# Performance work log

Measured on AMD Instinct MI355X. Metric: run time of the kernel, lower is better.

The kernel has to match this reference:

```python
import jax, jax.numpy as jnp
import numpy as np

B, S, K, D, H, COND, MR = 4, 1024, 1024, 1024, 16, 1024, 4
HD = D // H  # 64
INV_SQRT_HD = 1.0 / float(np.sqrt(HD))
GELU_C = 0.7978845608028654  # sqrt(2/pi)


def _make_rope(seqlen):
    pos = jnp.arange(seqlen, dtype=jnp.float32)
    inv = 1.0 / (10000.0 ** (jnp.arange(0, HD // 2, dtype=jnp.float32) * 2.0 / HD))
    ang = pos[:, None] * inv[None, :]                     # [S, HD/2]
    cos = jnp.concatenate([jnp.cos(ang), jnp.cos(ang)], -1)  # [S, HD]
    sin = jnp.concatenate([jnp.sin(ang), jnp.sin(ang)], -1)
    return cos[None, :, None, :], sin[None, :, None, :]   # [1,S,1,HD]


def setup_inputs():
    key = jax.random.key(0)
    ks = jax.random.split(key, 14)
    rn = lambda k, shape, s=0.02: jax.random.normal(k, shape, jnp.float32) * s
    cos_q, sin_q = _make_rope(S)
    cos_k, sin_k = _make_rope(K)
    ada_b = jnp.zeros((6 * D,), jnp.float32)
    ada_b = ada_b.at[2 * D:3 * D].set(0.5).at[5 * D:6 * D].set(0.5)  # gate_msa, gate_mlp init
    return {
        "q_x": jax.random.normal(ks[0], (B, S, D), jnp.float32),
        "kv_x": jax.random.normal(ks[1], (B, K, D), jnp.float32),
        "t_cond": jax.random.normal(ks[2], (B, COND), jnp.float32),
        "cos_q": cos_q, "sin_q": sin_q, "cos_k": cos_k, "sin_k": sin_k,
        "group_idxs": jax.random.randint(ks[3], (B, S), 0, 4, jnp.int32),
        "query_enabled": jax.random.randint(ks[4], (B, S), 0, 2, jnp.int32).astype(bool),
        "qn_w": jnp.ones((D,), jnp.float32),
        "kvn_w": jnp.ones((D,), jnp.float32),
        "n2_w": jnp.ones((D,), jnp.float32),
        "Wq": rn(ks[5], (D, D)), "Wkv": rn(ks[6], (D, 2 * D)), "Wo": rn(ks[7], (D, D)),
        "W1": rn(ks[8], (D, MR * D)), "b1": jnp.zeros((MR * D,), jnp.float32),
        "W2": rn(ks[9], (MR * D, D)), "b2": jnp.zeros((D,), jnp.float32),
        "adaW": rn(ks[10], (COND, 6 * D)), "adab": ada_b,
    }


def layer_norm(x, w):
    mu = jnp.mean(x, -1, keepdims=True)
    var = jnp.var(x, -1, keepdims=True)
    return (x - mu) * jax.lax.rsqrt(var + 1e-5) * w


def rope(x, cos, sin):
    # x: [B,S,H,HD]; cos/sin: [1,S,1,HD]; rotate_half convention
    x1, x2 = jnp.split(x, 2, axis=-1)
    return x * cos + jnp.concatenate([-x2, x1], -1) * sin


def gelu_tanh(x):
    return 0.5 * x * (1.0 + jnp.tanh(GELU_C * (x + 0.044715 * x * x * x)))


def reference(q_x, kv_x, t_cond, cos_q, sin_q, cos_k, sin_k, group_idxs, query_enabled,
              qn_w, kvn_w, n2_w, Wq, Wkv, Wo, W1, b1, W2, b2, adaW, adab):
    # adaLN modulation (inference: dropout disabled -> bias_dropout_add_scale = scale*x + residual)
    mod = (t_cond @ adaW + adab)[:, None, :]               # [B,1,6D]
    sh_msa, sc_msa, g_msa, sh_mlp, sc_mlp, g_mlp = jnp.split(mod, 6, axis=-1)

    qn = layer_norm(q_x, qn_w)
    kvn = layer_norm(kv_x, kvn_w)
    qn = qn * (1.0 + sc_msa) + sh_msa                      # modulate_fused

    q = (qn @ Wq).reshape(B, S, H, HD)
    kv = (kvn @ Wkv).reshape(B, K, 2, H, HD)
    k, v = kv[:, :, 0], kv[:, :, 1]
    q = rope(q, cos_q, sin_q)
    k = rope(k, cos_k, sin_k)

    # group cross-attn mask: attend only where groups differ
    attend = group_idxs[:, :, None] != group_idxs[:, None, :]  # [B,S,K]
    scores = jnp.einsum('bqhd,bkhd->bhqk', q, k) * INV_SQRT_HD
    scores = jnp.where(attend[:, None, :, :], scores, -1e9)
    p = jax.nn.softmax(scores, axis=-1)
    attn = jnp.einsum('bhqk,bkhd->bqhd', p, v).reshape(B, S, D)

    x = g_msa * (attn @ Wo) + q_x                          # fused bias-dropout-add-scale (inference)
    gate = query_enabled[..., None].astype(x.dtype)
    x = x * gate + q_x * (1.0 - gate)                      # gated_update

    x_mid = x
    h = layer_norm(x, n2_w) * (1.0 + sc_mlp) + sh_mlp
    h = gelu_tanh(h @ W1 + b1) @ W2 + b2
    x = g_mlp * h + x_mid
    x = x * gate + x_mid * (1.0 - gate)
    return x
```

## Files before the change

kernel.cpp:

```cpp
#include <hip/hip_runtime.h>
#include <hip/hip_bf16.h>
#include <math.h>

typedef __bf16 bf16_t;
typedef __attribute__((ext_vector_type(8))) __bf16 bf16x8;
typedef __attribute__((ext_vector_type(4))) __bf16 bf16x4;
typedef __attribute__((ext_vector_type(4))) float f32x4;

__global__ __launch_bounds__(256) void mod_init_kernel(
    const float* __restrict__ adab, float* __restrict__ mod)
{
  int i = blockIdx.x * 256 + threadIdx.x;
  int c = i % 6144;
  mod[i] = adab[c];
}

__global__ __launch_bounds__(256) void mod_partial_kernel(
    const float* __restrict__ tc, const float* __restrict__ adaW,
    float* __restrict__ mod)
{
  __shared__ float st[4][128];
  int tid = threadIdx.x, z = blockIdx.y;
  for (int i = tid; i < 512; i += 256)
    st[i >> 7][i & 127] = tc[(i >> 7) * 1024 + z * 128 + (i & 127)];
  __syncthreads();
  int col = blockIdx.x * 256 + tid;
  float a0 = 0.f, a1 = 0.f, a2 = 0.f, a3 = 0.f;
  for (int k = 0; k < 128; ++k) {
    float wv = adaW[(size_t)(z * 128 + k) * 6144 + col];
    a0 = fmaf(st[0][k], wv, a0);
    a1 = fmaf(st[1][k], wv, a1);
    a2 = fmaf(st[2][k], wv, a2);
    a3 = fmaf(st[3][k], wv, a3);
  }
  atomicAdd(&mod[col], a0);
  atomicAdd(&mod[6144 + col], a1);
  atomicAdd(&mod[2 * 6144 + col], a2);
  atomicAdd(&mod[3 * 6144 + col], a3);
}

__global__ __launch_bounds__(256) void transpose_to_bf16(
    const float* __restrict__ in, bf16_t* __restrict__ out, int R, int C)
{
  __shared__ float tile[32][33];
  int c0 = blockIdx.x * 32, r0 = blockIdx.y * 32;
  int tx = threadIdx.x, ty = threadIdx.y;
#pragma unroll
  for (int i = 0; i < 4; ++i)
    tile[ty + i * 8][tx] = in[(size_t)(r0 + ty + i * 8) * C + c0 + tx];
  __syncthreads();
#pragma unroll
  for (int i = 0; i < 4; ++i)
    out[(size_t)(c0 + ty + i * 8) * R + r0 + tx] = (bf16_t)tile[tx][ty + i * 8];
}

__global__ __launch_bounds__(256) void ln_mod_kernel(
    const float* __restrict__ x, const float* __restrict__ wgt,
    const float* __restrict__ mod, int useMod, int shOff, int scOff,
    bf16_t* __restrict__ out)
{
  int row = blockIdx.x;
  int b = row >> 10;
  int tid = threadIdx.x;
  const float* xr = x + (size_t)row * 1024;
  float4 v = ((const float4*)xr)[tid];
  float s = v.x + v.y + v.z + v.w;
  float s2 = v.x * v.x + v.y * v.y + v.z * v.z + v.w * v.w;
#pragma unroll
  for (int off = 32; off > 0; off >>= 1) {
    s += __shfl_down(s, off, 64);
    s2 += __shfl_down(s2, off, 64);
  }
  __shared__ float ps[4], ps2[4];
  if ((tid & 63) == 0) { ps[tid >> 6] = s; ps2[tid >> 6] = s2; }
  __syncthreads();
  float mu = (ps[0] + ps[1] + ps[2] + ps[3]) * (1.0f / 1024.0f);
  float var = (ps2[0] + ps2[1] + ps2[2] + ps2[3]) * (1.0f / 1024.0f) - mu * mu;
  float rs = rsqrtf(var + 1e-5f);
  float xv[4] = {v.x, v.y, v.z, v.w};
#pragma unroll
  for (int i = 0; i < 4; ++i) {
    int col = tid * 4 + i;
    float n = (xv[i] - mu) * rs * wgt[col];
    if (useMod)
      n = n * (1.0f + mod[b * 6144 + scOff + col]) + mod[b * 6144 + shOff + col];
    out[(size_t)row * 1024 + col] = (bf16_t)n;
  }
}

__global__ __launch_bounds__(256) void reduce_q_rope_kernel(
    const bf16_t* __restrict__ P0, const bf16_t* __restrict__ P1,
    const float* __restrict__ cosq, const float* __restrict__ sinq,
    bf16_t* __restrict__ qr)
{
  int t = blockIdx.x * 256 + threadIdx.x;
  int hd = t & 31;
  int h = (t >> 5) & 15;
  int s = (t >> 9) & 1023;
  int b = t >> 19;
  size_t base = ((size_t)(b * 1024 + s)) * 1024 + h * 64 + hd;
  float v1 = (float)P0[base] + (float)P1[base];
  float v2 = (float)P0[base + 32] + (float)P1[base + 32];
  float c1 = cosq[s * 64 + hd], s1 = sinq[s * 64 + hd];
  float c2 = cosq[s * 64 + hd + 32], s2 = sinq[s * 64 + hd + 32];
  float o1 = (v1 * c1 - v2 * s1) * 0.125f;
  float o2 = (v2 * c2 + v1 * s2) * 0.125f;
  size_t ob = ((size_t)(b * 16 + h) * 1024 + s) * 64 + hd;
  qr[ob] = (bf16_t)o1;
  qr[ob + 32] = (bf16_t)o2;
}

__global__ __launch_bounds__(256) void reduce_kv_kernel(
    const bf16_t* __restrict__ P0, const bf16_t* __restrict__ P1,
    const float* __restrict__ cosk, const float* __restrict__ sink,
    bf16_t* __restrict__ kr, bf16_t* __restrict__ vt)
{
  __shared__ float ks[64][65];
  __shared__ float vs[64][65];
  int bh = blockIdx.x;
  int b = bh >> 4, h = bh & 15;
  int n0 = blockIdx.y * 64;
  int tid = threadIdx.x;
#pragma unroll
  for (int it = 0; it < 16; ++it) {
    int linear = tid + it * 256;
    int nl = linear >> 6, hd = linear & 63;
    size_t gi = ((size_t)(b * 1024 + n0 + nl)) * 2048 + h * 64 + hd;
    ks[nl][hd] = (float)P0[gi] + (float)P1[gi];
    vs[hd][nl] = (float)P0[gi + 1024] + (float)P1[gi + 1024];
  }
  __syncthreads();
#pragma unroll
  for (int it = 0; it < 16; ++it) {
    int linear = tid + it * 256;
    int nl = linear >> 6, hd = linear & 63;
    float kv = ks[nl][hd];
    float pv = ks[nl][hd ^ 32];
    float c = cosk[(n0 + nl) * 64 + hd], sn = sink[(n0 + nl) * 64 + hd];
    float o = (hd < 32) ? (kv * c - pv * sn) : (kv * c + pv * sn);
    kr[((size_t)bh * 1024 + n0 + nl) * 64 + hd] = (bf16_t)o;
    int rh = linear >> 6, nn = linear & 63;
    vt[((size_t)bh * 64 + rh) * 1024 + n0 + nn] = (bf16_t)vs[rh][nn];
  }
}

__global__ __launch_bounds__(256, 2) void attn_kernel(
    const bf16_t* __restrict__ qr, const bf16_t* __restrict__ kr,
    const bf16_t* __restrict__ vt, const int* __restrict__ grp,
    bf16_t* __restrict__ outp)
{
  __shared__ bf16_t Ks[64 * 72];
  __shared__ bf16_t Vs[64 * 72];
  __shared__ bf16_t Ps[128 * 72];
  __shared__ int gk[64];
  const int bh = blockIdx.x;
  const int b = bh >> 4, h = bh & 15;
  const int qBase = blockIdx.y * 128;
  const int tid = threadIdx.x, lane = tid & 63, w = tid >> 6;
  const int l15 = lane & 15, l4 = lane >> 4;
  const f32x4 zero = {0.f, 0.f, 0.f, 0.f};

  bf16x8 qA0[2], qA1[2];
  int gqr[2][4];
#pragma unroll
  for (int s = 0; s < 2; ++s) {
    int row = qBase + w * 32 + s * 16;
    const bf16_t* qp = qr + ((size_t)bh * 1024 + row + l15) * 64;
    qA0[s] = *(const bf16x8*)(qp + l4 * 8);
    qA1[s] = *(const bf16x8*)(qp + 32 + l4 * 8);
#pragma unroll
    for (int r = 0; r < 4; ++r) gqr[s][r] = grp[b * 1024 + row + l4 * 4 + r];
  }

  f32x4 oacc[2][4];
  float rsum[2][4];
#pragma unroll
  for (int s = 0; s < 2; ++s)
#pragma unroll
    for (int i = 0; i < 4; ++i) { oacc[s][i] = zero; rsum[s][i] = 0.f; }

  for (int kt = 0; kt < 16; ++kt) {
    __syncthreads();
#pragma unroll
    for (int i = 0; i < 2; ++i) {
      int c = tid * 2 + i;
      int r = c >> 3, cc = (c & 7) * 8;
      *(bf16x8*)(Ks + r * 72 + cc) =
          *(const bf16x8*)(kr + ((size_t)bh * 1024 + kt * 64 + r) * 64 + cc);
      *(bf16x8*)(Vs + r * 72 + cc) =
          *(const bf16x8*)(vt + ((size_t)bh * 64 + r) * 1024 + kt * 64 + cc);
    }
    if (tid < 64) gk[tid] = grp[b * 1024 + kt * 64 + tid];
    __syncthreads();

    int gkv[4];
    bf16x8 kf0[4], kf1[4];
#pragma unroll
    for (int nt = 0; nt < 4; ++nt) {
      gkv[nt] = gk[nt * 16 + l15];
      kf0[nt] = *(const bf16x8*)(Ks + (nt * 16 + l15) * 72 + l4 * 8);
      kf1[nt] = *(const bf16x8*)(Ks + (nt * 16 + l15) * 72 + 32 + l4 * 8);
    }

#pragma unroll
    for (int s = 0; s < 2; ++s) {
      f32x4 sacc[4];
#pragma unroll
      for (int nt = 0; nt < 4; ++nt) sacc[nt] = zero;
#pragma unroll
      for (int nt = 0; nt < 4; ++nt) {
        sacc[nt] = __builtin_amdgcn_mfma_f32_16x16x32_bf16(qA0[s], kf0[nt], sacc[nt], 0, 0, 0);
        sacc[nt] = __builtin_amdgcn_mfma_f32_16x16x32_bf16(qA1[s], kf1[nt], sacc[nt], 0, 0, 0);
      }
#pragma unroll
      for (int r = 0; r < 4; ++r) {
        int gq = gqr[s][r];
        float acc = 0.f;
#pragma unroll
        for (int nt = 0; nt < 4; ++nt) {
          float sv = sacc[nt][r] + ((gq == gkv[nt]) ? -60.f : 0.f);
          float p = __expf(sv);
          acc += p;
          Ps[(w * 32 + s * 16 + l4 * 4 + r) * 72 + nt * 16 + l15] = (bf16_t)p;
        }
        rsum[s][r] += acc;
      }
    }
#pragma unroll
    for (int s = 0; s < 2; ++s) {
      const bf16_t* pp = Ps + (w * 32 + s * 16 + l15) * 72;
      bf16x8 pf0 = *(const bf16x8*)(pp + l4 * 8);
      bf16x8 pf1 = *(const bf16x8*)(pp + 32 + l4 * 8);
#pragma unroll
      for (int nt = 0; nt < 4; ++nt) {
        bf16x8 vf0 = *(const bf16x8*)(Vs + (nt * 16 + l15) * 72 + l4 * 8);
        bf16x8 vf1 = *(const bf16x8*)(Vs + (nt * 16 + l15) * 72 + 32 + l4 * 8);
        oacc[s][nt] = __builtin_amdgcn_mfma_f32_16x16x32_bf16(pf0, vf0, oacc[s][nt], 0, 0, 0);
        oacc[s][nt] = __builtin_amdgcn_mfma_f32_16x16x32_bf16(pf1, vf1, oacc[s][nt], 0, 0, 0);
      }
    }
  }

#pragma unroll
  for (int s = 0; s < 2; ++s)
#pragma unroll
    for (int r = 0; r < 4; ++r) {
      float t = rsum[s][r];
      t += __shfl_xor(t, 1, 64);
      t += __shfl_xor(t, 2, 64);
      t += __shfl_xor(t, 4, 64);
      t += __shfl_xor(t, 8, 64);
      rsum[s][r] = 1.f / t;
    }
#pragma unroll
  for (int s = 0; s < 2; ++s)
#pragma unroll
    for (int r = 0; r < 4; ++r) {
      int srow = qBase + w * 32 + s * 16 + l4 * 4 + r;
      float inv = rsum[s][r];
#pragma unroll
      for (int nt = 0; nt < 4; ++nt)
        outp[((size_t)(b * 1024 + srow)) * 1024 + h * 64 + nt * 16 + l15] =
            (bf16_t)(oacc[s][nt][r] * inv);
    }
}

__device__ __forceinline__ void stage16(const bf16_t* gp, bf16_t* lp) {
  __builtin_amdgcn_global_load_lds(
      (__attribute__((address_space(1))) void*)gp,
      (__attribute__((address_space(3))) void*)lp, 16, 0, 0);
}

template <int EPI>
__global__ __launch_bounds__(256, 2) void gemm_bt(
    const bf16_t* __restrict__ A, const bf16_t* __restrict__ Bt,
    int M, int N, int Kd, int kChunk,
    bf16_t* __restrict__ Cb,
    const float* __restrict__ bias)
{
  __shared__ bf16_t sA[128 * 64];
  __shared__ bf16_t sB[128 * 64];
  const int tid = threadIdx.x;
  const int lane = tid & 63, w = tid >> 6;
  const int wr = w >> 1, wc = w & 1;

  const int gx = gridDim.x, gy = gridDim.y;
  const int L = blockIdx.y * gx + blockIdx.x;
  const int xcd = L & 7, idx = L >> 3;
  const int ry = gy >> 2, rx = gx >> 1;
  const int tileY = (xcd & 3) * ry + (idx % ry);
  const int tileX = (xcd >> 2) * rx + (idx / ry);
  const int rowBase = tileY * 128;
  const int colBase = tileX * 128;

  const int l15 = lane & 15, l4 = lane >> 4;
  const int srow = lane >> 3;
  const int sg = lane & 7;
  const int scol = (sg ^ srow) * 8;
  const int rl = l15 & 7;
  const int g0 = (l4 ^ rl) * 8;
  const int g1 = ((4 + l4) ^ rl) * 8;

  const f32x4 zero = {0.f, 0.f, 0.f, 0.f};
  f32x4 acc[4][4];
#pragma unroll
  for (int i = 0; i < 4; ++i)
#pragma unroll
    for (int j = 0; j < 4; ++j) acc[i][j] = zero;

  const bf16_t* aBase = A + (size_t)(rowBase + w * 32 + srow) * Kd + scol;
  const bf16_t* bBase = Bt + (size_t)(colBase + w * 32 + srow) * Kd + scol;

  const int kStart = blockIdx.z * kChunk;
  for (int k0 = kStart; k0 < kStart + kChunk; k0 += 64) {
    __syncthreads();
#pragma unroll
    for (int i = 0; i < 4; ++i) {
      stage16(aBase + (size_t)i * 8 * Kd + k0, sA + (w * 32 + i * 8) * 64);
      stage16(bBase + (size_t)i * 8 * Kd + k0, sB + (w * 32 + i * 8) * 64);
    }
    __syncthreads();
    bf16x8 af[4], bfr[4];
#pragma unroll
    for (int mt = 0; mt < 4; ++mt)
      af[mt] = *(const bf16x8*)(sA + (wr * 64 + mt * 16 + l15) * 64 + g0);
#pragma unroll
    for (int nt = 0; nt < 4; ++nt)
      bfr[nt] = *(const bf16x8*)(sB + (wc * 64 + nt * 16 + l15) * 64 + g0);
#pragma unroll
    for (int mt = 0; mt < 4; ++mt)
#pragma unroll
      for (int nt = 0; nt < 4; ++nt)
        acc[mt][nt] = __builtin_amdgcn_mfma_f32_16x16x32_bf16(af[mt], bfr[nt],
                                                              acc[mt][nt], 0, 0, 0);
#pragma unroll
    for (int mt = 0; mt < 4; ++mt)
      af[mt] = *(const bf16x8*)(sA + (wr * 64 + mt * 16 + l15) * 64 + g1);
#pragma unroll
    for (int nt = 0; nt < 4; ++nt)
      bfr[nt] = *(const bf16x8*)(sB + (wc * 64 + nt * 16 + l15) * 64 + g1);
#pragma unroll
    for (int mt = 0; mt < 4; ++mt)
#pragma unroll
      for (int nt = 0; nt < 4; ++nt)
        acc[mt][nt] = __builtin_amdgcn_mfma_f32_16x16x32_bf16(af[mt], bfr[nt],
                                                              acc[mt][nt], 0, 0, 0);
  }

  const size_t zOff = (size_t)blockIdx.z * M * N;
#pragma unroll
  for (int mt = 0; mt < 4; ++mt) {
#pragma unroll
    for (int nt = 0; nt < 4; ++nt) {
      int col = colBase + wc * 64 + nt * 16 + l15;
#pragma unroll
      for (int r = 0; r < 4; ++r) {
        int rr = rowBase + wr * 64 + mt * 16 + l4 * 4 + r;
        float v = acc[mt][nt][r];
        if constexpr (EPI == 1) {
          float t = v + bias[col];
          float z = 0.7978845608028654f * (t + 0.044715f * t * t * t);
          float e = __expf(2.f * z);
          float g = 0.5f * t * (2.f - 2.f / (e + 1.f));
          Cb[(size_t)rr * N + col] = (bf16_t)g;
        } else {
          Cb[zOff + (size_t)rr * N + col] = (bf16_t)v;
        }
      }
    }
  }
}

__global__ __launch_bounds__(256) void ln2_fused_kernel(
    const bf16_t* __restrict__ P0, const bf16_t* __restrict__ P1,
    const float* __restrict__ qx, const float* __restrict__ n2w,
    const float* __restrict__ mod, const int* __restrict__ qen,
    float* __restrict__ xbuf, bf16_t* __restrict__ xnmod)
{
  int row = blockIdx.x;
  int b = row >> 10;
  int tid = threadIdx.x;
  bool en = qen[row] != 0;
  bf16x4 p0 = *(const bf16x4*)(P0 + (size_t)row * 1024 + tid * 4);
  bf16x4 p1 = *(const bf16x4*)(P1 + (size_t)row * 1024 + tid * 4);
  float4 res = ((const float4*)(qx + (size_t)row * 1024))[tid];
  float4 g = ((const float4*)(mod + b * 6144 + 2048))[tid];
  float4 x;
  x.x = en ? fmaf(g.x, (float)p0[0] + (float)p1[0], res.x) : res.x;
  x.y = en ? fmaf(g.y, (float)p0[1] + (float)p1[1], res.y) : res.y;
  x.z = en ? fmaf(g.z, (float)p0[2] + (float)p1[2], res.z) : res.z;
  x.w = en ? fmaf(g.w, (float)p0[3] + (float)p1[3], res.w) : res.w;
  ((float4*)(xbuf + (size_t)row * 1024))[tid] = x;

  float s = x.x + x.y + x.z + x.w;
  float s2 = x.x * x.x + x.y * x.y + x.z * x.z + x.w * x.w;
#pragma unroll
  for (int off = 32; off > 0; off >>= 1) {
    s += __shfl_down(s, off, 64);
    s2 += __shfl_down(s2, off, 64);
  }
  __shared__ float ps[4], ps2[4];
  if ((tid & 63) == 0) { ps[tid >> 6] = s; ps2[tid >> 6] = s2; }
  __syncthreads();
  float mu = (ps[0] + ps[1] + ps[2] + ps[3]) * (1.0f / 1024.0f);
  float var = (ps2[0] + ps2[1] + ps2[2] + ps2[3]) * (1.0f / 1024.0f) - mu * mu;
  float rs = rsqrtf(var + 1e-5f);
  float4 sc = ((const float4*)(mod + b * 6144 + 4096))[tid];
  float4 sh = ((const float4*)(mod + b * 6144 + 3072))[tid];
  float4 wv = ((const float4*)n2w)[tid];
  float xv[4] = {x.x, x.y, x.z, x.w};
  float scv[4] = {sc.x, sc.y, sc.z, sc.w};
  float shv[4] = {sh.x, sh.y, sh.z, sh.w};
  float wvv[4] = {wv.x, wv.y, wv.z, wv.w};
#pragma unroll
  for (int i = 0; i < 4; ++i) {
    float n = (xv[i] - mu) * rs * wvv[i];
    n = n * (1.0f + scv[i]) + shv[i];
    xnmod[(size_t)row * 1024 + tid * 4 + i] = (bf16_t)n;
  }
}

__global__ __launch_bounds__(256) void final_reduce_kernel(
    const bf16_t* __restrict__ P, const float* __restrict__ b2,
    const float* __restrict__ mod, const int* __restrict__ qen,
    const float* __restrict__ xbuf, float* __restrict__ out)
{
  int row = blockIdx.x;
  int b = row >> 10;
  int tid = threadIdx.x;
  bool en = qen[row] != 0;
  size_t ro = (size_t)row * 1024 + tid * 4;
  bf16x4 p0 = *(const bf16x4*)(P + ro);
  bf16x4 p1 = *(const bf16x4*)(P + 4194304 + ro);
  bf16x4 p2 = *(const bf16x4*)(P + 2 * 4194304 + ro);
  bf16x4 p3 = *(const bf16x4*)(P + 3 * 4194304 + ro);
  float4 bb = ((const float4*)b2)[tid];
  float4 xm = *(const float4*)(xbuf + ro);
  float4 g = ((const float4*)(mod + b * 6144 + 5120))[tid];
  float4 o;
  float v0 = (float)p0[0] + (float)p1[0] + (float)p2[0] + (float)p3[0] + bb.x;
  float v1 = (float)p0[1] + (float)p1[1] + (float)p2[1] + (float)p3[1] + bb.y;
  float v2 = (float)p0[2] + (float)p1[2] + (float)p2[2] + (float)p3[2] + bb.z;
  float v3 = (float)p0[3] + (float)p1[3] + (float)p2[3] + (float)p3[3] + bb.w;
  o.x = en ? fmaf(g.x, v0, xm.x) : xm.x;
  o.y = en ? fmaf(g.y, v1, xm.y) : xm.y;
  o.z = en ? fmaf(g.z, v2, xm.z) : xm.z;
  o.w = en ? fmaf(g.w, v3, xm.w) : xm.w;
  *(float4*)(out + ro) = o;
}

extern "C" void kernel_launch(void* const* d_in, const int* in_sizes, int n_in,
                              void* d_out, int out_size, void* d_ws, size_t ws_size,
                              hipStream_t stream)
{
  const float* q_x    = (const float*)d_in[0];
  const float* kv_x   = (const float*)d_in[1];
  const float* t_cond = (const float*)d_in[2];
  const float* cos_q  = (const float*)d_in[3];
  const float* sin_q  = (const float*)d_in[4];
  const float* cos_k  = (const float*)d_in[5];
  const float* sin_k  = (const float*)d_in[6];
  const int*   grp    = (const int*)d_in[7];
  const int*   qen    = (const int*)d_in[8];
  const float* qn_w   = (const float*)d_in[9];
  const float* kvn_w  = (const float*)d_in[10];
  const float* n2_w   = (const float*)d_in[11];
  const float* Wq     = (const float*)d_in[12];
  const float* Wkv    = (const float*)d_in[13];
  const float* Wo     = (const float*)d_in[14];
  const float* W1     = (const float*)d_in[15];
  const float* b1     = (const float*)d_in[16];
  const float* W2     = (const float*)d_in[17];
  const float* b2     = (const float*)d_in[18];
  const float* adaW   = (const float*)d_in[19];
  const float* adab   = (const float*)d_in[20];
  float* out = (float*)d_out;

  char* ws = (char*)d_ws;
  const size_t MB = 1ull << 20;
  float*  mod    = (float*)(ws + 0);
  bf16_t* Wq_t   = (bf16_t*)(ws + 98304);
  bf16_t* Wkv_t  = (bf16_t*)(ws + 98304 + 2 * MB);
  bf16_t* Wo_t   = (bf16_t*)(ws + 98304 + 6 * MB);
  bf16_t* W1_t   = (bf16_t*)(ws + 98304 + 8 * MB);
  bf16_t* W2_t   = (bf16_t*)(ws + 98304 + 16 * MB);
  bf16_t* qn_mod = (bf16_t*)(ws + 98304 + 24 * MB);
  bf16_t* kvn    = (bf16_t*)(ws + 98304 + 32 * MB);
  bf16_t* q_r    = (bf16_t*)(ws + 98304 + 40 * MB);
  bf16_t* k_r    = (bf16_t*)(ws + 98304 + 48 * MB);
  bf16_t* v_t    = (bf16_t*)(ws + 98304 + 56 * MB);
  bf16_t* h1     = (bf16_t*)(ws + 98304 + 64 * MB);
  bf16_t* scr    = (bf16_t*)(ws + 98304 + 96 * MB);
  bf16_t* xn_mod = qn_mod;
  bf16_t* attn_o = kvn;
  float*  xbuf   = (float*)q_r;

  mod_init_kernel<<<96, 256, 0, stream>>>(adab, mod);
  mod_partial_kernel<<<dim3(24, 8), 256, 0, stream>>>(t_cond, adaW, mod);
  transpose_to_bf16<<<dim3(32, 32),  dim3(32, 8), 0, stream>>>(Wq,  Wq_t,  1024, 1024);
  transpose_to_bf16<<<dim3(64, 32),  dim3(32, 8), 0, stream>>>(Wkv, Wkv_t, 1024, 2048);
  transpose_to_bf16<<<dim3(32, 32),  dim3(32, 8), 0, stream>>>(Wo,  Wo_t,  1024, 1024);
  transpose_to_bf16<<<dim3(128, 32), dim3(32, 8), 0, stream>>>(W1,  W1_t,  1024, 4096);
  transpose_to_bf16<<<dim3(32, 128), dim3(32, 8), 0, stream>>>(W2,  W2_t,  4096, 1024);
  ln_mod_kernel<<<4096, 256, 0, stream>>>(q_x,  qn_w,  mod, 1, 0, 1024, qn_mod);
  ln_mod_kernel<<<4096, 256, 0, stream>>>(kv_x, kvn_w, mod, 0, 0, 0,    kvn);
  gemm_bt<4><<<dim3(8, 32, 2), 256, 0, stream>>>(qn_mod, Wq_t, 4096, 1024, 1024, 512,
                                                 scr, nullptr);
  reduce_q_rope_kernel<<<8192, 256, 0, stream>>>(scr, scr + 4194304, cos_q, sin_q, q_r);
  gemm_bt<4><<<dim3(16, 32, 2), 256, 0, stream>>>(kvn, Wkv_t, 4096, 2048, 1024, 512,
                                                  scr, nullptr);
  reduce_kv_kernel<<<dim3(64, 16), 256, 0, stream>>>(scr, scr + 8388608, cos_k, sin_k,
                                                     k_r, v_t);
  attn_kernel<<<dim3(64, 8), 256, 0, stream>>>(q_r, k_r, v_t, grp, attn_o);
  gemm_bt<4><<<dim3(8, 32, 2), 256, 0, stream>>>(attn_o, Wo_t, 4096, 1024, 1024, 512,
                                                 scr, nullptr);
  ln2_fused_kernel<<<4096, 256, 0, stream>>>(scr, scr + 4194304, q_x, n2_w, mod, qen,
                                             xbuf, xn_mod);
  gemm_bt<1><<<dim3(32, 32, 1), 256, 0, stream>>>(xn_mod, W1_t, 4096, 4096, 1024, 1024,
                                                  h1, b1);
  gemm_bt<4><<<dim3(8, 32, 4), 256, 0, stream>>>(h1, W2_t, 4096, 1024, 4096, 1024,
                                                 scr, nullptr);
  final_reduce_kernel<<<4096, 256, 0, stream>>>(scr, b2, mod, qen, xbuf, out);
}
```

Measured before the change: 436.5 us.

## Compact enabled query rows and skip post-attention GEMMs for disabled rows

Adds a compaction kernel that builds an index list of rows with query_enabled set. The Wo projection gathers only those rows, and the LN2 and MLP GEMMs run on the compacted rows, with blocks past the live count exiting early. Disabled rows are copied straight from q_x into the output. The change also merges the five weight transposes and the two layer norms into single launches and changes the Wo split-K to 4. The intent is to avoid GEMM work on rows whose result is discarded, at the cost of a serial single-block scan and an indirect row gather.

After: 397.3 us. 1.1x faster.

```diff
diff --git a/kernel.cpp b/kernel.cpp
--- a/kernel.cpp
+++ b/kernel.cpp
@@ -7,12 +7,51 @@
 typedef __attribute__((ext_vector_type(4))) __bf16 bf16x4;
 typedef __attribute__((ext_vector_type(4))) float f32x4;
 
+__global__ __launch_bounds__(256) void compact_kernel(
+    const int* __restrict__ qen, int* __restrict__ idx, int* __restrict__ McPtr)
+{
+  __shared__ int cnts[256];
+  int t = threadIdx.x;
+  int flags[16], c = 0;
+#pragma unroll
+  for (int i = 0; i < 16; ++i) {
+    flags[i] = qen[t * 16 + i] != 0;
+    c += flags[i];
+  }
+  cnts[t] = c;
+  __syncthreads();
+  for (int off = 1; off < 256; off <<= 1) {
+    int v = cnts[t];
+    if (t >= off) v += cnts[t - off];
+    __syncthreads();
+    cnts[t] = v;
+    __syncthreads();
+  }
+  int p = cnts[t] - c;
+  int total = cnts[255];
+#pragma unroll
+  for (int i = 0; i < 16; ++i)
+    if (flags[i]) idx[p++] = t * 16 + i;
+  if (t == 0) *McPtr = total;
+  for (int j = total + t; j < 4096; j += 256) idx[j] = 0;
+}
+
+__global__ __launch_bounds__(256) void copy_disabled_kernel(
+    const int* __restrict__ qen, const float* __restrict__ qx,
+    float* __restrict__ out)
+{
+  int row = blockIdx.x;
+  if (qen[row]) return;
+  int tid = threadIdx.x;
+  ((float4*)(out + (size_t)row * 1024))[tid] =
+      ((const float4*)(qx + (size_t)row * 1024))[tid];
+}
+
 __global__ __launch_bounds__(256) void mod_init_kernel(
     const float* __restrict__ adab, float* __restrict__ mod)
 {
   int i = blockIdx.x * 256 + threadIdx.x;
-  int c = i % 6144;
-  mod[i] = adab[c];
+  mod[i] = adab[i % 6144];
 }
 
 __global__ __launch_bounds__(256) void mod_partial_kernel(
@@ -39,11 +78,23 @@
   atomicAdd(&mod[3 * 6144 + col], a3);
 }
 
-__global__ __launch_bounds__(256) void transpose_to_bf16(
-    const float* __restrict__ in, bf16_t* __restrict__ out, int R, int C)
+__global__ __launch_bounds__(256) void transpose_all(
+    const float* __restrict__ Wq, const float* __restrict__ Wkv,
+    const float* __restrict__ Wo, const float* __restrict__ W1,
+    const float* __restrict__ W2,
+    bf16_t* __restrict__ oWq, bf16_t* __restrict__ oWkv,
+    bf16_t* __restrict__ oWo, bf16_t* __restrict__ oW1,
+    bf16_t* __restrict__ oW2)
 {
   __shared__ float tile[32][33];
-  int c0 = blockIdx.x * 32, r0 = blockIdx.y * 32;
+  int bid = blockIdx.x;
+  const float* in; bf16_t* out; int R, C, gx, local;
+  if (bid < 1024)      { in = Wq;  out = oWq;  R = 1024; C = 1024; gx = 32;  local = bid; }
+  else if (bid < 3072) { in = Wkv; out = oWkv; R = 1024; C = 2048; gx = 64;  local = bid - 1024; }
+  else if (bid < 4096) { in = Wo;  out = oWo;  R = 1024; C = 1024; gx = 32;  local = bid - 3072; }
+  else if (bid < 8192) { in = W1;  out = oW1;  R = 1024; C = 4096; gx = 128; local = bid - 4096; }
+  else                 { in = W2;  out = oW2;  R = 4096; C = 1024; gx = 32;  local = bid - 8192; }
+  int c0 = (local % gx) * 32, r0 = (local / gx) * 32;
   int tx = threadIdx.x, ty = threadIdx.y;
 #pragma unroll
   for (int i = 0; i < 4; ++i)
@@ -54,16 +105,22 @@
     out[(size_t)(c0 + ty + i * 8) * R + r0 + tx] = (bf16_t)tile[tx][ty + i * 8];
 }
 
-__global__ __launch_bounds__(256) void ln_mod_kernel(
-    const float* __restrict__ x, const float* __restrict__ wgt,
-    const float* __restrict__ mod, int useMod, int shOff, int scOff,
-    bf16_t* __restrict__ out)
-{
-  int row = blockIdx.x;
+__global__ __launch_bounds__(256) void ln_both_kernel(
+    const float* __restrict__ qx, const float* __restrict__ kvx,
+    const float* __restrict__ qnw, const float* __restrict__ kvnw,
+    const float* __restrict__ mod,
+    bf16_t* __restrict__ qn_out, bf16_t* __restrict__ kvn_out)
+{
+  int rowg = blockIdx.x;
+  bool isQ = rowg < 4096;
+  int row = isQ ? rowg : rowg - 4096;
   int b = row >> 10;
   int tid = threadIdx.x;
-  const float* xr = x + (size_t)row * 1024;
-  float4 v = ((const float4*)xr)[tid];
+  const float* x = (isQ ? qx : kvx) + (size_t)row * 1024;
+  const float* wgt = isQ ? qnw : kvnw;
+  bf16_t* outp = (isQ ? qn_out : kvn_out) + (size_t)row * 1024;
+
+  float4 v = ((const float4*)x)[tid];
   float s = v.x + v.y + v.z + v.w;
   float s2 = v.x * v.x + v.y * v.y + v.z * v.z + v.w * v.w;
 #pragma unroll
@@ -82,9 +139,9 @@
   for (int i = 0; i < 4; ++i) {
     int col = tid * 4 + i;
     float n = (xv[i] - mu) * rs * wgt[col];
-    if (useMod)
-      n = n * (1.0f + mod[b * 6144 + scOff + col]) + mod[b * 6144 + shOff + col];
-    out[(size_t)row * 1024 + col] = (bf16_t)n;
+    if (isQ)
+      n = n * (1.0f + mod[b * 6144 + 1024 + col]) + mod[b * 6144 + col];
+    outp[col] = (bf16_t)n;
   }
 }
 
@@ -139,8 +196,7 @@
     float c = cosk[(n0 + nl) * 64 + hd], sn = sink[(n0 + nl) * 64 + hd];
     float o = (hd < 32) ? (kv * c - pv * sn) : (kv * c + pv * sn);
     kr[((size_t)bh * 1024 + n0 + nl) * 64 + hd] = (bf16_t)o;
-    int rh = linear >> 6, nn = linear & 63;
-    vt[((size_t)bh * 64 + rh) * 1024 + n0 + nn] = (bf16_t)vs[rh][nn];
+    vt[((size_t)bh * 64 + nl) * 1024 + n0 + hd] = (bf16_t)vs[nl][hd];
   }
 }
 
@@ -271,12 +327,9 @@
       (__attribute__((address_space(3))) void*)lp, 16, 0, 0);
 }
 
-template <int EPI>
-__global__ __launch_bounds__(256, 2) void gemm_bt(
+__global__ __launch_bounds__(256, 2) void gemm_bt_full(
     const bf16_t* __restrict__ A, const bf16_t* __restrict__ Bt,
-    int M, int N, int Kd, int kChunk,
-    bf16_t* __restrict__ Cb,
-    const float* __restrict__ bias)
+    int M, int N, int Kd, int kChunk, bf16_t* __restrict__ Cb)
 {
   __shared__ bf16_t sA[128 * 64];
   __shared__ bf16_t sB[128 * 64];
@@ -286,10 +339,10 @@
 
   const int gx = gridDim.x, gy = gridDim.y;
   const int L = blockIdx.y * gx + blockIdx.x;
-  const int xcd = L & 7, idx = L >> 3;
+  const int xcd = L & 7, id2 = L >> 3;
   const int ry = gy >> 2, rx = gx >> 1;
-  const int tileY = (xcd & 3) * ry + (idx % ry);
-  const int tileX = (xcd >> 2) * rx + (idx / ry);
+  const int tileY = (xcd & 3) * ry + (id2 % ry);
+  const int tileX = (xcd >> 2) * rx + (id2 / ry);
   const int rowBase = tileY * 128;
   const int colBase = tileX * 128;
 
@@ -349,7 +402,103 @@
 
   const size_t zOff = (size_t)blockIdx.z * M * N;
 #pragma unroll
-  for (int mt = 0; mt < 4; ++mt) {
+  for (int mt = 0; mt < 4; ++mt)
+#pragma unroll
+    for (int nt = 0; nt < 4; ++nt) {
+      int col = colBase + wc * 64 + nt * 16 + l15;
+#pragma unroll
+      for (int r = 0; r < 4; ++r) {
+        int rr = rowBase + wr * 64 + mt * 16 + l4 * 4 + r;
+        Cb[zOff + (size_t)rr * N + col] = (bf16_t)acc[mt][nt][r];
+      }
+    }
+}
+
+template <int EPI, int GATHER>
+__global__ __launch_bounds__(256, 2) void gemm_bt_c(
+    const bf16_t* __restrict__ A, const bf16_t* __restrict__ Bt,
+    int N, int Kd, int kChunk, bf16_t* __restrict__ Cb,
+    const float* __restrict__ bias,
+    const int* __restrict__ idxG, const int* __restrict__ McPtr)
+{
+  __shared__ bf16_t sA[128 * 64];
+  __shared__ bf16_t sB[128 * 64];
+  const int Mc = *McPtr;
+  const int gx = gridDim.x;
+  const int L = blockIdx.y * gx + blockIdx.x;
+  const int xcd = L & 7, id2 = L >> 3;
+  const int tileY = (id2 / gx) * 8 + xcd;
+  const int tileX = id2 % gx;
+  const int rowBase = tileY * 128;
+  if (rowBase >= Mc) return;
+  const int colBase = tileX * 128;
+
+  const int tid = threadIdx.x;
+  const int lane = tid & 63, w = tid >> 6;
+  const int wr = w >> 1, wc = w & 1;
+  const int l15 = lane & 15, l4 = lane >> 4;
+  const int srow = lane >> 3;
+  const int sg = lane & 7;
+  const int scol = (sg ^ srow) * 8;
+  const int rl = l15 & 7;
+  const int g0 = (l4 ^ rl) * 8;
+  const int g1 = ((4 + l4) ^ rl) * 8;
+
+  const f32x4 zero = {0.f, 0.f, 0.f, 0.f};
+  f32x4 acc[4][4];
+#pragma unroll
+  for (int i = 0; i < 4; ++i)
+#pragma unroll
+    for (int j = 0; j < 4; ++j) acc[i][j] = zero;
+
+  const bf16_t* aB[4];
+#pragma unroll
+  for (int i = 0; i < 4; ++i) {
+    int rowc = rowBase + w * 32 + i * 8 + srow;
+    int arow = GATHER ? idxG[rowc] : rowc;
+    aB[i] = A + (size_t)arow * Kd + scol;
+  }
+  const bf16_t* bBase = Bt + (size_t)(colBase + w * 32 + srow) * Kd + scol;
+
+  const int kStart = blockIdx.z * kChunk;
+  for (int k0 = kStart; k0 < kStart + kChunk; k0 += 64) {
+    __syncthreads();
+#pragma unroll
+    for (int i = 0; i < 4; ++i) {
+      stage16(aB[i] + k0, sA + (w * 32 + i * 8) * 64);
+      stage16(bBase + (size_t)i * 8 * Kd + k0, sB + (w * 32 + i * 8) * 64);
+    }
+    __syncthreads();
+    bf16x8 af[4], bfr[4];
+#pragma unroll
+    for (int mt = 0; mt < 4; ++mt)
+      af[mt] = *(const bf16x8*)(sA + (wr * 64 + mt * 16 + l15) * 64 + g0);
+#pragma unroll
+    for (int nt = 0; nt < 4; ++nt)
+      bfr[nt] = *(const bf16x8*)(sB + (wc * 64 + nt * 16 + l15) * 64 + g0);
+#pragma unroll
+    for (int mt = 0; mt < 4; ++mt)
+#pragma unroll
+      for (int nt = 0; nt < 4; ++nt)
+        acc[mt][nt] = __builtin_amdgcn_mfma_f32_16x16x32_bf16(af[mt], bfr[nt],
+                                                              acc[mt][nt], 0, 0, 0);
+#pragma unroll
+    for (int mt = 0; mt < 4; ++mt)
+      af[mt] = *(const bf16x8*)(sA + (wr * 64 + mt * 16 + l15) * 64 + g1);
+#pragma unroll
+    for (int nt = 0; nt < 4; ++nt)
+      bfr[nt] = *(const bf16x8*)(sB + (wc * 64 + nt * 16 + l15) * 64 + g1);
+#pragma unroll
+    for (int mt = 0; mt < 4; ++mt)
+#pragma unroll
+      for (int nt = 0; nt < 4; ++nt)
+        acc[mt][nt] = __builtin_amdgcn_mfma_f32_16x16x32_bf16(af[mt], bfr[nt],
+                                                              acc[mt][nt], 0, 0, 0);
+  }
+
+  const size_t zOff = (size_t)blockIdx.z * 4096 * N;
+#pragma unroll
+  for (int mt = 0; mt < 4; ++mt)
 #pragma unroll
     for (int nt = 0; nt < 4; ++nt) {
       int col = colBase + wc * 64 + nt * 16 + l15;
@@ -368,29 +517,32 @@
         }
       }
     }
-  }
 }
 
 __global__ __launch_bounds__(256) void ln2_fused_kernel(
-    const bf16_t* __restrict__ P0, const bf16_t* __restrict__ P1,
-    const float* __restrict__ qx, const float* __restrict__ n2w,
-    const float* __restrict__ mod, const int* __restrict__ qen,
-    float* __restrict__ xbuf, bf16_t* __restrict__ xnmod)
-{
-  int row = blockIdx.x;
-  int b = row >> 10;
+    const bf16_t* __restrict__ P, const float* __restrict__ qx,
+    const float* __restrict__ n2w, const float* __restrict__ mod,
+    const int* __restrict__ idxG, const int* __restrict__ McPtr,
+    float* __restrict__ xbufc, bf16_t* __restrict__ xnc)
+{
+  int rowc = blockIdx.x;
+  if (rowc >= *McPtr) return;
+  int rr = idxG[rowc];
+  int b = rr >> 10;
   int tid = threadIdx.x;
-  bool en = qen[row] != 0;
-  bf16x4 p0 = *(const bf16x4*)(P0 + (size_t)row * 1024 + tid * 4);
-  bf16x4 p1 = *(const bf16x4*)(P1 + (size_t)row * 1024 + tid * 4);
-  float4 res = ((const float4*)(qx + (size_t)row * 1024))[tid];
+  size_t rc = (size_t)rowc * 1024 + tid * 4;
+  bf16x4 p0 = *(const bf16x4*)(P + rc);
+  bf16x4 p1 = *(const bf16x4*)(P + 4194304 + rc);
+  bf16x4 p2 = *(const bf16x4*)(P + 2 * 4194304 + rc);
+  bf16x4 p3 = *(const bf16x4*)(P + 3 * 4194304 + rc);
+  float4 res = ((const float4*)(qx + (size_t)rr * 1024))[tid];
   float4 g = ((const float4*)(mod + b * 6144 + 2048))[tid];
   float4 x;
-  x.x = en ? fmaf(g.x, (float)p0[0] + (float)p1[0], res.x) : res.x;
-  x.y = en ? fmaf(g.y, (float)p0[1] + (float)p1[1], res.y) : res.y;
-  x.z = en ? fmaf(g.z, (float)p0[2] + (float)p1[2], res.z) : res.z;
-  x.w = en ? fmaf(g.w, (float)p0[3] + (float)p1[3], res.w) : res.w;
-  ((float4*)(xbuf + (size_t)row * 1024))[tid] = x;
+  x.x = fmaf(g.x, (float)p0[0] + (float)p1[0] + (float)p2[0] + (float)p3[0], res.x);
+  x.y = fmaf(g.y, (float)p0[1] + (float)p1[1] + (float)p2[1] + (float)p3[1], res.y);
+  x.z = fmaf(g.z, (float)p0[2] + (float)p1[2] + (float)p2[2] + (float)p3[2], res.z);
+  x.w = fmaf(g.w, (float)p0[3] + (float)p1[3] + (float)p2[3] + (float)p3[3], res.w);
+  *(float4*)(xbufc + rc) = x;
 
   float s = x.x + x.y + x.z + x.w;
   float s2 = x.x * x.x + x.y * x.y + x.z * x.z + x.w * x.w;
@@ -416,37 +568,39 @@
   for (int i = 0; i < 4; ++i) {
     float n = (xv[i] - mu) * rs * wvv[i];
     n = n * (1.0f + scv[i]) + shv[i];
-    xnmod[(size_t)row * 1024 + tid * 4 + i] = (bf16_t)n;
+    xnc[(size_t)rowc * 1024 + tid * 4 + i] = (bf16_t)n;
   }
 }
 
 __global__ __launch_bounds__(256) void final_reduce_kernel(
     const bf16_t* __restrict__ P, const float* __restrict__ b2,
-    const float* __restrict__ mod, const int* __restrict__ qen,
-    const float* __restrict__ xbuf, float* __restrict__ out)
-{
-  int row = blockIdx.x;
-  int b = row >> 10;
+    const float* __restrict__ mod, const int* __restrict__ idxG,
+    const int* __restrict__ McPtr, const float* __restrict__ xbufc,
+    float* __restrict__ out)
+{
+  int rowc = blockIdx.x;
+  if (rowc >= *McPtr) return;
+  int rr = idxG[rowc];
+  int b = rr >> 10;
   int tid = threadIdx.x;
-  bool en = qen[row] != 0;
-  size_t ro = (size_t)row * 1024 + tid * 4;
-  bf16x4 p0 = *(const bf16x4*)(P + ro);
-  bf16x4 p1 = *(const bf16x4*)(P + 4194304 + ro);
-  bf16x4 p2 = *(const bf16x4*)(P + 2 * 4194304 + ro);
-  bf16x4 p3 = *(const bf16x4*)(P + 3 * 4194304 + ro);
+  size_t rc = (size_t)rowc * 1024 + tid * 4;
+  bf16x4 p0 = *(const bf16x4*)(P + rc);
+  bf16x4 p1 = *(const bf16x4*)(P + 4194304 + rc);
+  bf16x4 p2 = *(const bf16x4*)(P + 2 * 4194304 + rc);
+  bf16x4 p3 = *(const bf16x4*)(P + 3 * 4194304 + rc);
   float4 bb = ((const float4*)b2)[tid];
-  float4 xm = *(const float4*)(xbuf + ro);
+  float4 xm = *(const float4*)(xbufc + rc);
   float4 g = ((const float4*)(mod + b * 6144 + 5120))[tid];
-  float4 o;
   float v0 = (float)p0[0] + (float)p1[0] + (float)p2[0] + (float)p3[0] + bb.x;
   float v1 = (float)p0[1] + (float)p1[1] + (float)p2[1] + (float)p3[1] + bb.y;
   float v2 = (float)p0[2] + (float)p1[2] + (float)p2[2] + (float)p3[2] + bb.z;
   float v3 = (float)p0[3] + (float)p1[3] + (float)p2[3] + (float)p3[3] + bb.w;
-  o.x = en ? fmaf(g.x, v0, xm.x) : xm.x;
-  o.y = en ? fmaf(g.y, v1, xm.y) : xm.y;
-  o.z = en ? fmaf(g.z, v2, xm.z) : xm.z;
-  o.w = en ? fmaf(g.w, v3, xm.w) : xm.w;
-  *(float4*)(out + ro) = o;
+  float4 o;
+  o.x = fmaf(g.x, v0, xm.x);
+  o.y = fmaf(g.y, v1, xm.y);
+  o.z = fmaf(g.z, v2, xm.z);
+  o.w = fmaf(g.w, v3, xm.w);
+  *(float4*)(out + (size_t)rr * 1024 + tid * 4) = o;
 }
 
 extern "C" void kernel_launch(void* const* d_in, const int* in_sizes, int n_in,
@@ -479,46 +633,48 @@
   char* ws = (char*)d_ws;
   const size_t MB = 1ull << 20;
   float*  mod    = (float*)(ws + 0);
-  bf16_t* Wq_t   = (bf16_t*)(ws + 98304);
-  bf16_t* Wkv_t  = (bf16_t*)(ws + 98304 + 2 * MB);
-  bf16_t* Wo_t   = (bf16_t*)(ws + 98304 + 6 * MB);
-  bf16_t* W1_t   = (bf16_t*)(ws + 98304 + 8 * MB);
-  bf16_t* W2_t   = (bf16_t*)(ws + 98304 + 16 * MB);
-  bf16_t* qn_mod = (bf16_t*)(ws + 98304 + 24 * MB);
-  bf16_t* kvn    = (bf16_t*)(ws + 98304 + 32 * MB);
-  bf16_t* q_r    = (bf16_t*)(ws + 98304 + 40 * MB);
-  bf16_t* k_r    = (bf16_t*)(ws + 98304 + 48 * MB);
-  bf16_t* v_t    = (bf16_t*)(ws + 98304 + 56 * MB);
-  bf16_t* h1     = (bf16_t*)(ws + 98304 + 64 * MB);
-  bf16_t* scr    = (bf16_t*)(ws + 98304 + 96 * MB);
-  bf16_t* xn_mod = qn_mod;
+  int*    idxL   = (int*)(ws + 98304);
+  int*    McPtr  = (int*)(ws + 98304 + 16384);
+  char*   wbase  = ws + 131072;
+  bf16_t* Wq_t   = (bf16_t*)(wbase);
+  bf16_t* Wkv_t  = (bf16_t*)(wbase + 2 * MB);
+  bf16_t* Wo_t   = (bf16_t*)(wbase + 6 * MB);
+  bf16_t* W1_t   = (bf16_t*)(wbase + 8 * MB);
+  bf16_t* W2_t   = (bf16_t*)(wbase + 16 * MB);
+  bf16_t* qn_mod = (bf16_t*)(wbase + 24 * MB);
+  bf16_t* kvn    = (bf16_t*)(wbase + 32 * MB);
+  bf16_t* q_r    = (bf16_t*)(wbase + 40 * MB);
+  bf16_t* k_r    = (bf16_t*)(wbase + 48 * MB);
+  bf16_t* v_t    = (bf16_t*)(wbase + 56 * MB);
+  bf16_t* h1     = (bf16_t*)(wbase + 64 * MB);
+  bf16_t* scr    = (bf16_t*)(wbase + 96 * MB);
+  bf16_t* xn_c   = qn_mod;
   bf16_t* attn_o = kvn;
-  float*  xbuf   = (float*)q_r;
-
+  float*  xbuf_c = (float*)q_r;
+
+  compact_kernel<<<1, 256, 0, stream>>>(qen, idxL, McPtr);
+  copy_disabled_kernel<<<4096, 256, 0, stream>>>(qen, q_x, out);
   mod_init_kernel<<<96, 256, 0, stream>>>(adab, mod);
   mod_partial_kernel<<<dim3(24, 8), 256, 0, stream>>>(t_cond, adaW, mod);
-  transpose_to_bf16<<<dim3(32, 32),  dim3(32, 8), 0, stream>>>(Wq,  Wq_t,  1024, 1024);
-  transpose_to_bf16<<<dim3(64, 32),  dim3(32, 8), 0, stream>>>(Wkv, Wkv_t, 1024, 2048);
-  transpose_to_bf16<<<dim3(32, 32),  dim3(32, 8), 0, stream>>>(Wo,  Wo_t,  1024, 1024);
-  transpose_to_bf16<<<dim3(128, 32), dim3(32, 8), 0, stream>>>(W1,  W1_t,  1024, 4096);
-  transpose_to_bf16<<<dim3(32, 128), dim3(32, 8), 0, stream>>>(W2,  W2_t,  4096, 1024);
-  ln_mod_kernel<<<4096, 256, 0, stream>>>(q_x,  qn_w,  mod, 1, 0, 1024, qn_mod);
-  ln_mod_kernel<<<4096, 256, 0, stream>>>(kv_x, kvn_w, mod, 0, 0, 0,    kvn);
-  gemm_bt<4><<<dim3(8, 32, 2), 256, 0, stream>>>(qn_mod, Wq_t, 4096, 1024, 1024, 512,
-                                                 scr, nullptr);
+  transpose_all<<<12288, dim3(32, 8), 0, stream>>>(Wq, Wkv, Wo, W1, W2,
+                                                   Wq_t, Wkv_t, Wo_t, W1_t, W2_t);
+  ln_both_kernel<<<8192, 256, 0, stream>>>(q_x, kv_x, qn_w, kvn_w, mod,
+                                           qn_mod, kvn);
+  gemm_bt_full<<<dim3(8, 32, 2), 256, 0, stream>>>(qn_mod, Wq_t, 4096, 1024, 1024,
+                                                   512, scr);
   reduce_q_rope_kernel<<<8192, 256, 0, stream>>>(scr, scr + 4194304, cos_q, sin_q, q_r);
-  gemm_bt<4><<<dim3(16, 32, 2), 256, 0, stream>>>(kvn, Wkv_t, 4096, 2048, 1024, 512,
-                                                  scr, nullptr);
+  gemm_bt_full<<<dim3(16, 32, 2), 256, 0, stream>>>(kvn, Wkv_t, 4096, 2048, 1024,
+                                                    512, scr);
   reduce_kv_kernel<<<dim3(64, 16), 256, 0, stream>>>(scr, scr + 8388608, cos_k, sin_k,
                                                      k_r, v_t);
   attn_kernel<<<dim3(64, 8), 256, 0, stream>>>(q_r, k_r, v_t, grp, attn_o);
-  gemm_bt<4><<<dim3(8, 32, 2), 256, 0, stream>>>(attn_o, Wo_t, 4096, 1024, 1024, 512,
-                                                 scr, nullptr);
-  ln2_fused_kernel<<<4096, 256, 0, stream>>>(scr, scr + 4194304, q_x, n2_w, mod, qen,
-                                             xbuf, xn_mod);
-  gemm_bt<1><<<dim3(32, 32, 1), 256, 0, stream>>>(xn_mod, W1_t, 4096, 4096, 1024, 1024,
-                                                  h1, b1);
-  gemm_bt<4><<<dim3(8, 32, 4), 256, 0, stream>>>(h1, W2_t, 4096, 1024, 4096, 1024,
-                                                 scr, nullptr);
-  final_reduce_kernel<<<4096, 256, 0, stream>>>(scr, b2, mod, qen, xbuf, out);
-}
+  gemm_bt_c<4, 1><<<dim3(8, 32, 4), 256, 0, stream>>>(attn_o, Wo_t, 1024, 1024, 256,
+                                                      scr, nullptr, idxL, McPtr);
+  ln2_fused_kernel<<<4096, 256, 0, stream>>>(scr, q_x, n2_w, mod, idxL, McPtr,
+                                             xbuf_c, xn_c);
+  gemm_bt_c<1, 0><<<dim3(32, 32, 1), 256, 0, stream>>>(xn_c, W1_t, 4096, 1024, 1024,
+                                                       h1, b1, idxL, McPtr);
+  gemm_bt_c<4, 0><<<dim3(8, 32, 4), 256, 0, stream>>>(h1, W2_t, 1024, 4096, 1024,
+                                                      scr, nullptr, idxL, McPtr);
+  final_reduce_kernel<<<4096, 256, 0, stream>>>(scr, b2, mod, idxL, McPtr, xbuf_c, out);
+}
```
